# Kernel optimization log

Hardware: AMD Instinct MI355X
Metric: run time of the kernel (lower is better)

Reference implementation:

```python
import jax, jax.numpy as jnp
import numpy as np

B, T, E, H = 4, 512, 1024, 16
D = E // H  # 64
EPS = 1e-5  # torch LayerNorm default


def _ln(x, g, b):
    m = jnp.mean(x, axis=-1, keepdims=True)
    v = jnp.mean(jnp.square(x - m), axis=-1, keepdims=True)
    return (x - m) * jax.lax.rsqrt(v + EPS) * g + b


def _multihead(x, wq, wk, wv, g, b, mask):
    # x: [B,T,E]; wq/wk/wv: [H,E,D]; g,b: [H,D]; mask: [T,T] bool (causal)
    q = jnp.einsum('bte,hed->bhtd', x, wq)
    k = jnp.einsum('bte,hed->bhtd', x, wk)
    v = jnp.einsum('bte,hed->bhtd', x, wv)
    aff = jnp.einsum('bhtd,bhsd->bhts', q, k)  # NOTE: no 1/sqrt(d) scaling, as in source
    aff = jnp.where(mask, aff, -jnp.inf)
    p = jax.nn.softmax(aff, axis=-1)
    o = jnp.einsum('bhts,bhsd->bhtd', p, v)
    o = _ln(o, g[None, :, None, :], b[None, :, None, :])  # per-head LayerNorm over D
    o = o.transpose(0, 2, 1, 3).reshape(B, T, E)  # concat heads
    return x + o


def _ff(x, w1, b1, w2, b2, g, bb):
    h = jnp.maximum(jnp.einsum('bte,ef->btf', x, w1) + b1, 0.0)
    h = jnp.einsum('btf,fe->bte', h, w2) + b2
    h = _ln(h, g, bb)
    return x + h


def setup_inputs() -> dict:
    key = jax.random.key(0)
    ks = jax.random.split(key, 8)
    s = 0.02
    return {
        'x': jax.random.normal(ks[0], (B, T, E), jnp.float32),
        'mh_wq': jax.random.normal(ks[1], (5, H, E, D), jnp.float32) * s,
        'mh_wk': jax.random.normal(ks[2], (5, H, E, D), jnp.float32) * s,
        'mh_wv': jax.random.normal(ks[3], (5, H, E, D), jnp.float32) * s,
        'mh_g': jnp.ones((5, H, D), jnp.float32),
        'mh_b': jnp.zeros((5, H, D), jnp.float32),
        'ff_w1': jax.random.normal(ks[4], (4, E, 4 * E), jnp.float32) * s,
        'ff_b1': jnp.zeros((4, 4 * E), jnp.float32),
        'ff_w2': jax.random.normal(ks[5], (4, 4 * E, E), jnp.float32) * s,
        'ff_b2': jnp.zeros((4, E), jnp.float32),
        'ff_g': jnp.ones((4, E), jnp.float32),
        'ff_bb': jnp.zeros((4, E), jnp.float32),
        'lt_w': jax.random.normal(ks[6], (2 * E, E), jnp.float32) * s,
        'lt_b': jnp.zeros((E,), jnp.float32),
    }


def reference(x, mh_wq, mh_wk, mh_wv, mh_g, mh_b,
              ff_w1, ff_b1, ff_w2, ff_b2, ff_g, ff_bb, lt_w, lt_b):
    mask = jnp.tril(jnp.ones((T, T), dtype=bool))

    def mh(i, y):
        return _multihead(y, mh_wq[i], mh_wk[i], mh_wv[i], mh_g[i], mh_b[i], mask)

    def ff(i, y):
        return _ff(y, ff_w1[i], ff_b1[i], ff_w2[i], ff_b2[i], ff_g[i], ff_bb[i])

    def decoder(y):  # MultiHeadwithEncoder + FeedForward (param sets 4 / 3)
        return ff(3, mh(4, y))

    # head_one branch
    out_one = decoder(mh(0, x))
    # encoder branch: 3 EncoderBlocks (MultiHead + FeedForward each)
    out_two = x
    for i in range(3):
        out_two = ff(i, mh(1 + i, out_two))
    out_two = decoder(out_two)

    out = jnp.concatenate([out_one, out_two], axis=-1)
    out = jnp.einsum('btf,fe->bte', out, lt_w) + lt_b
    # input; the result is identical each time, so computing it once is faithful.
    return out
```

## Files before the change

kernel.cpp:

```cpp
#include <hip/hip_runtime.h>
#include <math.h>

#define Bb 4
#define Tt 512
#define Ee 1024
#define Hh 16
#define Dd 64
#define Ff 4096
#define Mm (Bb*Tt)
static constexpr float EPS = 1e-5f;

typedef __attribute__((ext_vector_type(8))) short short8;
typedef __attribute__((ext_vector_type(4))) float f32x4;
typedef unsigned short u16;
typedef _Float16 f16;
typedef __attribute__((ext_vector_type(8))) _Float16 f16x8;

__device__ __forceinline__ u16 f2bf(float f) {
  unsigned u = __builtin_bit_cast(unsigned, f);
  return (u16)((u + 0x7fffu + ((u >> 16) & 1u)) >> 16);
}
__device__ __forceinline__ float bf2f(u16 h) {
  unsigned u = (unsigned)h << 16;
  return __builtin_bit_cast(float, u);
}
__device__ __forceinline__ void gload16(const void* g, void* l) {
  __builtin_amdgcn_global_load_lds(
      (const __attribute__((address_space(1))) unsigned int*)g,
      (__attribute__((address_space(3))) unsigned int*)l, 16, 0, 0);
}

__global__ __launch_bounds__(256)
void gemm_f16_128(const f16* __restrict__ A, const f16* __restrict__ W,
                  const float* __restrict__ bias,
                  f16* __restrict__ C, int ldc, int K)
{
  __shared__ f16 AS[128][32], BS[128][32];
  const int tid = threadIdx.x;
  const int lane = tid & 63, w = tid >> 6;
  const int wr = w >> 1, wc = w & 1;
  const int lhi = lane >> 4, llo = lane & 15;
  const int n0 = blockIdx.x * 128, m0 = blockIdx.y * 128;
  const int s_row = tid >> 2, s_ko = (tid & 3) * 8;

  f32x4 acc[4][4] = {};

  for (int k0 = 0; k0 < K; k0 += 32) {
#pragma unroll
    for (int i = 0; i < 2; ++i) {
      const int row = s_row + i * 64;
      gload16(&A[(size_t)(m0 + row) * K + k0 + s_ko], &AS[row][s_ko]);
      gload16(&W[(size_t)(n0 + row) * K + k0 + s_ko], &BS[row][s_ko]);
    }
    __syncthreads();
    f16x8 af[4], bf[4];
#pragma unroll
    for (int f = 0; f < 4; ++f) {
      af[f] = *(const f16x8*)&AS[wr * 64 + f * 16 + llo][lhi * 8];
      bf[f] = *(const f16x8*)&BS[wc * 64 + f * 16 + llo][lhi * 8];
    }
#pragma unroll
    for (int m = 0; m < 4; ++m)
#pragma unroll
      for (int n = 0; n < 4; ++n)
        acc[m][n] = __builtin_amdgcn_mfma_f32_16x16x32_f16(af[m], bf[n], acc[m][n], 0, 0, 0);
    __syncthreads();
  }

#pragma unroll
  for (int n = 0; n < 4; ++n) {
    const int col = n0 + wc * 64 + n * 16 + llo;
    const float bv = bias[col];
#pragma unroll
    for (int m = 0; m < 4; ++m) {
      const int rbase = m0 + wr * 64 + m * 16 + lhi * 4;
#pragma unroll
      for (int j = 0; j < 4; ++j) {
        float v = fmaxf(acc[m][n][j] + bv, 0.f);
        C[(size_t)(rbase + j) * ldc + col] = (f16)v;
      }
    }
  }
}

template<bool CONCAT>
__global__ __launch_bounds__(256)
void gemm_f16_1p(const f16* __restrict__ A, const f16* __restrict__ A2,
                 const f16* __restrict__ W,
                 float* __restrict__ Cf, float* __restrict__ Cf1,
                 int ldc, int K)
{
  __shared__ f16 AS[2][64][32], BS[2][128][32];
  const int tid = threadIdx.x;
  const int lane = tid & 63, w = tid >> 6;
  const int wr = w >> 1, wc = w & 1;
  const int lhi = lane >> 4, llo = lane & 15;
  const int n0 = blockIdx.x * 128;
  const int m0 = blockIdx.y * 64;
  const int half = K >> 1;
  const int kbeg = blockIdx.z * half;
  const int nt = half / 32;
  if (blockIdx.z == 1) Cf = Cf1;

  const int s_row = tid >> 2, s_ko = (tid & 3) * 8;

  auto stage = [&](int k0, int buf) {
    const int gk = k0 + s_ko;
    const f16* s = A;
    size_t g;
    if (CONCAT) {
      if (gk < Ee) { g = (size_t)(m0 + s_row) * Ee + gk; }
      else { g = (size_t)(m0 + s_row) * Ee + (gk - Ee); s = A2; }
    } else {
      g = (size_t)(m0 + s_row) * K + gk;
    }
    gload16(&s[g], &AS[buf][s_row][s_ko]);
#pragma unroll
    for (int i = 0; i < 2; ++i)
      gload16(&W[(size_t)(n0 + s_row + i * 64) * K + gk], &BS[buf][s_row + i * 64][s_ko]);
  };

  f32x4 acc[2][4] = {};
  stage(kbeg, 0);
  __syncthreads();
  int cur = 0;
  for (int t = 0; t < nt; ++t) {
    if (t + 1 < nt) stage(kbeg + (t + 1) * 32, cur ^ 1);
    f16x8 af[2], bf[4];
#pragma unroll
    for (int m = 0; m < 2; ++m)
      af[m] = *(const f16x8*)&AS[cur][wr * 32 + m * 16 + llo][lhi * 8];
#pragma unroll
    for (int n = 0; n < 4; ++n)
      bf[n] = *(const f16x8*)&BS[cur][wc * 64 + n * 16 + llo][lhi * 8];
#pragma unroll
    for (int m = 0; m < 2; ++m)
#pragma unroll
      for (int n = 0; n < 4; ++n)
        acc[m][n] = __builtin_amdgcn_mfma_f32_16x16x32_f16(af[m], bf[n], acc[m][n], 0, 0, 0);
    __syncthreads();
    cur ^= 1;
  }

#pragma unroll
  for (int n = 0; n < 4; ++n) {
    const int col = n0 + wc * 64 + n * 16 + llo;
#pragma unroll
    for (int m = 0; m < 2; ++m) {
      const int rbase = m0 + wr * 32 + m * 16 + lhi * 4;
#pragma unroll
      for (int j = 0; j < 4; ++j)
        Cf[(size_t)(rbase + j) * ldc + col] = acc[m][n][j];
    }
  }
}

__global__ __launch_bounds__(256)
void gemm_qkv(const f16* __restrict__ Ah_g, const f16* __restrict__ Al_g,
              const f16* __restrict__ Wh, const f16* __restrict__ Wl,
              float* __restrict__ Cq, float* __restrict__ Ck, float* __restrict__ Cv)
{
  __shared__ f16 AhS[2][64][32], AlS[2][64][32];
  __shared__ f16 BhS[2][128][32], BlS[2][128][32];
  const int tid = threadIdx.x;
  const int lane = tid & 63, w = tid >> 6;
  const int wr = w >> 1, wc = w & 1;
  const int lhi = lane >> 4, llo = lane & 15;
  const int sec = blockIdx.x >> 3;
  const int n0 = (blockIdx.x & 7) * 128;
  Wh += (size_t)sec << 20;
  Wl += (size_t)sec << 20;
  float* Cf = (sec == 0) ? Cq : (sec == 1) ? Ck : Cv;
  const int m0 = blockIdx.y * 64;
  const int s_row = tid >> 2, s_ko = (tid & 3) * 8;

  auto stage = [&](int k0, int buf) {
    const size_t g = (size_t)(m0 + s_row) * Ee + k0 + s_ko;
    gload16(&Ah_g[g], &AhS[buf][s_row][s_ko]);
    gload16(&Al_g[g], &AlS[buf][s_row][s_ko]);
#pragma unroll
    for (int i = 0; i < 2; ++i) {
      size_t gb = (size_t)(n0 + s_row + i * 64) * Ee + k0 + s_ko;
      gload16(&Wh[gb], &BhS[buf][s_row + i * 64][s_ko]);
      gload16(&Wl[gb], &BlS[buf][s_row + i * 64][s_ko]);
    }
  };

  f32x4 acc[2][4] = {};
  stage(0, 0);
  __syncthreads();
  int cur = 0;
  for (int t = 0; t < Ee / 32; ++t) {
    if (t + 1 < Ee / 32) stage((t + 1) * 32, cur ^ 1);
    f16x8 ah[2], al[2], bh[4], bl[4];
#pragma unroll
    for (int m = 0; m < 2; ++m) {
      ah[m] = *(const f16x8*)&AhS[cur][wr * 32 + m * 16 + llo][lhi * 8];
      al[m] = *(const f16x8*)&AlS[cur][wr * 32 + m * 16 + llo][lhi * 8];
    }
#pragma unroll
    for (int n = 0; n < 4; ++n) {
      bh[n] = *(const f16x8*)&BhS[cur][wc * 64 + n * 16 + llo][lhi * 8];
      bl[n] = *(const f16x8*)&BlS[cur][wc * 64 + n * 16 + llo][lhi * 8];
    }
#pragma unroll
    for (int m = 0; m < 2; ++m)
#pragma unroll
      for (int n = 0; n < 4; ++n) {
        acc[m][n] = __builtin_amdgcn_mfma_f32_16x16x32_f16(ah[m], bh[n], acc[m][n], 0, 0, 0);
        acc[m][n] = __builtin_amdgcn_mfma_f32_16x16x32_f16(ah[m], bl[n], acc[m][n], 0, 0, 0);
        acc[m][n] = __builtin_amdgcn_mfma_f32_16x16x32_f16(al[m], bh[n], acc[m][n], 0, 0, 0);
      }
    __syncthreads();
    cur ^= 1;
  }

#pragma unroll
  for (int n = 0; n < 4; ++n) {
    const int col = n0 + wc * 64 + n * 16 + llo;
#pragma unroll
    for (int m = 0; m < 2; ++m) {
      const int rbase = m0 + wr * 32 + m * 16 + lhi * 4;
#pragma unroll
      for (int j = 0; j < 4; ++j)
        Cf[(size_t)(rbase + j) * Ee + col] = acc[m][n][j];
    }
  }
}

__global__ __launch_bounds__(256)
void attn_ms(const float* __restrict__ Q, const float* __restrict__ Kp,
             const float* __restrict__ V, float* __restrict__ O)
{
  __shared__ u16 Ksh[64][72], Ksl[64][72];
  __shared__ u16 Vsh[64][72], Vsl[64][72];
  __shared__ u16 Pwh[4][16][72], Pwl[4][16][72];
  const int tid = threadIdx.x;
  const int lane = tid & 63, w = tid >> 6;
  const int lhi = lane >> 4, llo = lane & 15;
  const int q0 = blockIdx.x * 64;
  const int bh = blockIdx.y;
  const size_t base = (size_t)(bh >> 4) * Tt * Ee + (size_t)(bh & 15) * Dd;

  short8 qh[2], ql[2];
#pragma unroll
  for (int ks = 0; ks < 2; ++ks) {
    const float* qsrc = &Q[base + (size_t)(q0 + w * 16 + llo) * Ee + ks * 32 + lhi * 8];
    float4 a = *(const float4*)qsrc, b2 = *(const float4*)(qsrc + 4);
    float f[8] = {a.x, a.y, a.z, a.w, b2.x, b2.y, b2.z, b2.w};
#pragma unroll
    for (int j = 0; j < 8; ++j) {
      u16 h = f2bf(f[j]);
      qh[ks][j] = (short)h;
      ql[ks][j] = (short)f2bf(f[j] - bf2f(h));
    }
  }

  f32x4 oacc[4] = {};
  float m_run[4], l_run[4];
#pragma unroll
  for (int j = 0; j < 4; ++j) { m_run[j] = -INFINITY; l_run[j] = 0.f; }

  for (int s0 = 0; s0 <= q0; s0 += 64) {
#pragma unroll
    for (int pass = 0; pass < 2; ++pass) {
      int c = tid + 256 * pass;
      int row = c >> 3, d0 = (c & 7) * 8;
      const float* ksrc = &Kp[base + (size_t)(s0 + row) * Ee + d0];
      const float* vsrc = &V[base + (size_t)(s0 + row) * Ee + d0];
      float4 ka = *(const float4*)ksrc, kb2 = *(const float4*)(ksrc + 4);
      float4 va = *(const float4*)vsrc, vb2 = *(const float4*)(vsrc + 4);
      float kf[8] = {ka.x, ka.y, ka.z, ka.w, kb2.x, kb2.y, kb2.z, kb2.w};
      float vf[8] = {va.x, va.y, va.z, va.w, vb2.x, vb2.y, vb2.z, vb2.w};
      short8 khv, klv;
#pragma unroll
      for (int j = 0; j < 8; ++j) {
        u16 h = f2bf(kf[j]);
        khv[j] = (short)h;
        klv[j] = (short)f2bf(kf[j] - bf2f(h));
      }
      *(short8*)&Ksh[row][d0] = khv;
      *(short8*)&Ksl[row][d0] = klv;
#pragma unroll
      for (int j = 0; j < 8; ++j) {
        u16 h = f2bf(vf[j]);
        Vsh[d0 + j][row] = h;
        Vsl[d0 + j][row] = f2bf(vf[j] - bf2f(h));
      }
    }
    __syncthreads();

    f32x4 sacc[4] = {};
#pragma unroll
    for (int ks = 0; ks < 2; ++ks)
#pragma unroll
      for (int n = 0; n < 4; ++n) {
        short8 kh = *(const short8*)&Ksh[n * 16 + llo][ks * 32 + lhi * 8];
        short8 kl = *(const short8*)&Ksl[n * 16 + llo][ks * 32 + lhi * 8];
        sacc[n] = __builtin_amdgcn_mfma_f32_16x16x32_bf16(qh[ks], kh, sacc[n], 0, 0, 0);
        sacc[n] = __builtin_amdgcn_mfma_f32_16x16x32_bf16(qh[ks], kl, sacc[n], 0, 0, 0);
        sacc[n] = __builtin_amdgcn_mfma_f32_16x16x32_bf16(ql[ks], kh, sacc[n], 0, 0, 0);
      }

    if (s0 == q0) {
#pragma unroll
      for (int n = 0; n < 4; ++n)
#pragma unroll
        for (int j = 0; j < 4; ++j)
          if (n * 16 + llo > w * 16 + lhi * 4 + j) sacc[n][j] = -INFINITY;
    }

    float scj[4];
#pragma unroll
    for (int j = 0; j < 4; ++j) {
      float mt = fmaxf(fmaxf(sacc[0][j], sacc[1][j]), fmaxf(sacc[2][j], sacc[3][j]));
#pragma unroll
      for (int off = 1; off < 16; off <<= 1) mt = fmaxf(mt, __shfl_xor(mt, off));
      float mn = fmaxf(m_run[j], mt);
      scj[j] = __expf(m_run[j] - mn);
      m_run[j] = mn;
      float rs = 0.f;
#pragma unroll
      for (int n = 0; n < 4; ++n) {
        float pp = __expf(sacc[n][j] - mn);
        sacc[n][j] = pp;
        rs += pp;
      }
#pragma unroll
      for (int off = 1; off < 16; off <<= 1) rs += __shfl_xor(rs, off);
      l_run[j] = l_run[j] * scj[j] + rs;
    }

#pragma unroll
    for (int n = 0; n < 4; ++n)
#pragma unroll
      for (int j = 0; j < 4; ++j) {
        float pp = sacc[n][j];
        u16 h = f2bf(pp);
        Pwh[w][lhi * 4 + j][n * 16 + llo] = h;
        Pwl[w][lhi * 4 + j][n * 16 + llo] = f2bf(pp - bf2f(h));
      }
#pragma unroll
    for (int df = 0; df < 4; ++df)
#pragma unroll
      for (int j = 0; j < 4; ++j)
        oacc[df][j] *= scj[j];

#pragma unroll
    for (int ks = 0; ks < 2; ++ks) {
      short8 ph = *(const short8*)&Pwh[w][llo][ks * 32 + lhi * 8];
      short8 pl = *(const short8*)&Pwl[w][llo][ks * 32 + lhi * 8];
#pragma unroll
      for (int df = 0; df < 4; ++df) {
        short8 vh = *(const short8*)&Vsh[df * 16 + llo][ks * 32 + lhi * 8];
        short8 vl = *(const short8*)&Vsl[df * 16 + llo][ks * 32 + lhi * 8];
        oacc[df] = __builtin_amdgcn_mfma_f32_16x16x32_bf16(ph, vh, oacc[df], 0, 0, 0);
        oacc[df] = __builtin_amdgcn_mfma_f32_16x16x32_bf16(ph, vl, oacc[df], 0, 0, 0);
        oacc[df] = __builtin_amdgcn_mfma_f32_16x16x32_bf16(pl, vh, oacc[df], 0, 0, 0);
      }
    }
    __syncthreads();
  }

#pragma unroll
  for (int j = 0; j < 4; ++j) {
    float inv = 1.f / l_run[j];
#pragma unroll
    for (int df = 0; df < 4; ++df)
      O[base + (size_t)(q0 + w * 16 + lhi * 4 + j) * Ee + df * 16 + llo] =
          oacc[df][j] * inv;
  }
}

__global__ __launch_bounds__(256)
void attn_ln_res(const float* __restrict__ O, const float* __restrict__ Yin,
                 const float* __restrict__ g, const float* __restrict__ bta,
                 float* __restrict__ Yout, f16* __restrict__ Yh, f16* __restrict__ Yl)
{
  const int tid = threadIdx.x;
  const int w = (blockIdx.x << 2) + (tid >> 6);
  const int lane = tid & 63;
  const int m = w >> 4;
  const int h = w & 15;
  const size_t idx = (size_t)m * Ee + h * Dd + lane;
  float x = O[idx];
  float s = x, s2 = x * x;
#pragma unroll
  for (int off = 1; off < 64; off <<= 1) {
    s  += __shfl_xor(s, off);
    s2 += __shfl_xor(s2, off);
  }
  float mean = s * (1.f / 64.f);
  float var  = s2 * (1.f / 64.f) - mean * mean;
  float inv  = rsqrtf(var + EPS);
  float r = Yin[idx] + (x - mean) * inv * g[h * Dd + lane] + bta[h * Dd + lane];
  Yout[idx] = r;
  f16 hh = (f16)r;
  Yh[idx] = hh;
  Yl[idx] = (f16)(r - (float)hh);
}

__global__ __launch_bounds__(256)
void ff_ln_res(const float* __restrict__ T0, const float* __restrict__ T1,
               const float* __restrict__ b2,
               const float* __restrict__ Yin, const float* __restrict__ g,
               const float* __restrict__ bb,
               float* __restrict__ Yout, f16* __restrict__ Yh, f16* __restrict__ Yl)
{
  __shared__ float red[8];
  const int m = blockIdx.x;
  const int tid = threadIdx.x;
  const size_t basep = (size_t)m * Ee;
  float4 xa = *(const float4*)&T0[basep + (tid << 2)];
  float4 xb = *(const float4*)&T1[basep + (tid << 2)];
  float4 bv2 = *(const float4*)&b2[tid << 2];
  float xv[4] = {xa.x + xb.x + bv2.x, xa.y + xb.y + bv2.y,
                 xa.z + xb.z + bv2.z, xa.w + xb.w + bv2.w};
  float s  = xv[0] + xv[1] + xv[2] + xv[3];
  float s2 = xv[0]*xv[0] + xv[1]*xv[1] + xv[2]*xv[2] + xv[3]*xv[3];
#pragma unroll
  for (int off = 1; off < 64; off <<= 1) {
    s  += __shfl_xor(s, off);
    s2 += __shfl_xor(s2, off);
  }
  const int wid = tid >> 6;
  if ((tid & 63) == 0) { red[wid] = s; red[4 + wid] = s2; }
  __syncthreads();
  s  = red[0] + red[1] + red[2] + red[3];
  s2 = red[4] + red[5] + red[6] + red[7];
  float mean = s * (1.f / Ee);
  float var  = s2 * (1.f / Ee) - mean * mean;
  float inv  = rsqrtf(var + EPS);
  float4 y  = *(const float4*)&Yin[basep + (tid << 2)];
  float4 gg = *(const float4*)&g[tid << 2];
  float4 bv = *(const float4*)&bb[tid << 2];
  float gga[4] = {gg.x, gg.y, gg.z, gg.w};
  float bva[4] = {bv.x, bv.y, bv.z, bv.w};
  float ya[4] = {y.x, y.y, y.z, y.w};
  float o[4];
#pragma unroll
  for (int j = 0; j < 4; ++j) {
    o[j] = ya[j] + (xv[j] - mean) * inv * gga[j] + bva[j];
    f16 hh = (f16)o[j];
    Yh[basep + (tid << 2) + j] = hh;
    Yl[basep + (tid << 2) + j] = (f16)(o[j] - (float)hh);
  }
  *(float4*)&Yout[basep + (tid << 2)] = *(float4*)o;
}

__global__ __launch_bounds__(256)
void add2_bias(const float* __restrict__ p0, const float* __restrict__ p1,
               const float* __restrict__ b, float* __restrict__ out)
{
  const size_t i = ((size_t)blockIdx.x * 256 + threadIdx.x) * 4;
  const int col = (int)(i & (Ee - 1));
  float4 a = *(const float4*)&p0[i];
  float4 c = *(const float4*)&p1[i];
  float4 bb = *(const float4*)&b[col];
  float4 o;
  o.x = a.x + c.x + bb.x; o.y = a.y + c.y + bb.y;
  o.z = a.z + c.z + bb.z; o.w = a.w + c.w + bb.w;
  *(float4*)&out[i] = o;
}

__global__ __launch_bounds__(256)
void split_act(const float* __restrict__ in, f16* __restrict__ oh, f16* __restrict__ ol)
{
  const size_t i = ((size_t)blockIdx.x * 256 + threadIdx.x) * 4;
  float4 v = *(const float4*)&in[i];
  float f[4] = {v.x, v.y, v.z, v.w};
#pragma unroll
  for (int j = 0; j < 4; ++j) {
    f16 h = (f16)f[j];
    oh[i + j] = h;
    ol[i + j] = (f16)(f[j] - (float)h);
  }
}

__global__ __launch_bounds__(256)
void cvtT_f16(const float* __restrict__ in, f16* __restrict__ outp, int R, int C)
{
  __shared__ float tile[32][33];
  const int c0 = blockIdx.x * 32, r0 = blockIdx.y * 32;
  const int tid = threadIdx.x;
  const int ir = tid >> 3, ic = (tid & 7) * 4;
  float4 v = *(const float4*)&in[(size_t)(r0 + ir) * C + c0 + ic];
  tile[ir][ic] = v.x; tile[ir][ic + 1] = v.y;
  tile[ir][ic + 2] = v.z; tile[ir][ic + 3] = v.w;
  __syncthreads();
  const int oc = tid >> 3, orr = (tid & 7) * 4;
  const size_t ob = (size_t)(c0 + oc) * R + r0 + orr;
#pragma unroll
  for (int j = 0; j < 4; ++j)
    outp[ob + j] = (f16)tile[orr + j][oc];
}

__global__ __launch_bounds__(256)
void cvtT_qkv(const float* __restrict__ wq, const float* __restrict__ wk,
              const float* __restrict__ wv, f16* __restrict__ out_h,
              f16* __restrict__ out_l)
{
  __shared__ float tile[32][33];
  const int z = blockIdx.z, sec = z >> 4, hh = z & 15;
  const float* in = (sec == 0) ? wq : (sec == 1) ? wk : wv;
  const size_t zi = (size_t)hh * Ee * Dd;
  const size_t zo = ((size_t)sec << 20) + (size_t)hh * Ee * Dd;
  const int c0 = blockIdx.x * 32, r0 = blockIdx.y * 32;
  const int tid = threadIdx.x;
  const int ir = tid >> 3, ic = (tid & 7) * 4;
  float4 v = *(const float4*)&in[zi + (size_t)(r0 + ir) * Dd + c0 + ic];
  tile[ir][ic] = v.x; tile[ir][ic + 1] = v.y;
  tile[ir][ic + 2] = v.z; tile[ir][ic + 3] = v.w;
  __syncthreads();
  const int oc = tid >> 3, orr = (tid & 7) * 4;
  const size_t ob = zo + (size_t)(c0 + oc) * Ee + r0 + orr;
#pragma unroll
  for (int j = 0; j < 4; ++j) {
    float f = tile[orr + j][oc];
    f16 h = (f16)f;
    out_h[ob + j] = h;
    out_l[ob + j] = (f16)(f - (float)h);
  }
}

extern "C" void kernel_launch(void* const* d_in, const int* in_sizes, int n_in,
                              void* d_out, int out_size, void* d_ws, size_t ws_size,
                              hipStream_t stream)
{
  const float* x     = (const float*)d_in[0];
  const float* mh_wq = (const float*)d_in[1];
  const float* mh_wk = (const float*)d_in[2];
  const float* mh_wv = (const float*)d_in[3];
  const float* mh_g  = (const float*)d_in[4];
  const float* mh_b  = (const float*)d_in[5];
  const float* ff_w1 = (const float*)d_in[6];
  const float* ff_b1 = (const float*)d_in[7];
  const float* ff_w2 = (const float*)d_in[8];
  const float* ff_b2 = (const float*)d_in[9];
  const float* ff_g  = (const float*)d_in[10];
  const float* ff_bb = (const float*)d_in[11];
  const float* lt_w  = (const float*)d_in[12];
  const float* lt_b  = (const float*)d_in[13];
  float* out = (float*)d_out;

  const size_t ME = (size_t)Mm * Ee;
  char* p = (char*)d_ws;
  auto alloc = [&](size_t bytes) { void* r = (void*)p; p += (bytes + 255) & ~(size_t)255; return r; };
  float* bufA  = (float*)alloc(ME * 4);
  f16*   bufAh = (f16*)alloc(ME * 2);
  f16*   bufAl = (f16*)alloc(ME * 2);
  float* bufB  = (float*)alloc(ME * 4);
  f16*   bufBh = (f16*)alloc(ME * 2);
  f16*   bufBl = (f16*)alloc(ME * 2);
  f16*   wt_h  = (f16*)alloc((size_t)Ff * Ee * 2);
  f16*   wt_l  = (f16*)alloc((size_t)Ff * Ee * 2);
  float* reg   = (float*)alloc((size_t)10 * 1024 * 1024 * 4);
  float* qb    = reg;
  float* kb    = reg + 2 * 1024 * 1024;
  float* vb    = reg + 4 * 1024 * 1024;
  float* ob    = reg + 6 * 1024 * 1024;
  f16*   hid   = (f16*)reg;
  float* tmp   = reg + 8 * 1024 * 1024;

  auto mh = [&](int i, const float* srcF, const f16* srcH, const f16* srcL,
                float* dstF, f16* dstH, f16* dstL) {
    const size_t wo = (size_t)i * Hh * Ee * Dd;
    cvtT_qkv<<<dim3(Dd / 32, Ee / 32, 48), 256, 0, stream>>>(
        mh_wq + wo, mh_wk + wo, mh_wv + wo, wt_h, wt_l);
    gemm_qkv<<<dim3(24, Mm / 64), 256, 0, stream>>>(
        srcH, srcL, wt_h, wt_l, qb, kb, vb);
    attn_ms<<<dim3(Tt / 64, Bb * Hh), 256, 0, stream>>>(qb, kb, vb, ob);
    attn_ln_res<<<dim3(Mm * Hh / 4), 256, 0, stream>>>(
        ob, srcF, mh_g + (size_t)i * Hh * Dd, mh_b + (size_t)i * Hh * Dd, dstF, dstH, dstL);
  };
  auto ff = [&](int i, const float* srcF, const f16* srcH,
                float* dstF, f16* dstH, f16* dstL, float* tmp1) {
    cvtT_f16<<<dim3(Ff / 32, Ee / 32), 256, 0, stream>>>(ff_w1 + (size_t)i * Ee * Ff, wt_h, Ee, Ff);
    gemm_f16_128<<<dim3(Ff / 128, Mm / 128), 256, 0, stream>>>(
        srcH, wt_h, ff_b1 + (size_t)i * Ff, hid, Ff, Ee);
    cvtT_f16<<<dim3(Ee / 32, Ff / 32), 256, 0, stream>>>(ff_w2 + (size_t)i * Ff * Ee, wt_h, Ff, Ee);
    gemm_f16_1p<false><<<dim3(Ee / 128, Mm / 64, 2), 256, 0, stream>>>(
        hid, nullptr, wt_h, tmp, tmp1, Ee, Ff);
    ff_ln_res<<<dim3(Mm), 256, 0, stream>>>(
        tmp, tmp1, ff_b2 + (size_t)i * Ee,
        srcF, ff_g + (size_t)i * Ee, ff_bb + (size_t)i * Ee, dstF, dstH, dstL);
  };

  split_act<<<dim3(ME / 1024), 256, 0, stream>>>(x, bufAh, bufAl);
  mh(0, x, bufAh, bufAl, bufA, bufAh, bufAl);
  mh(4, bufA, bufAh, bufAl, bufA, bufAh, bufAl);
  ff(3, bufA, bufAh, bufA, bufAh, bufAl, bufB);

  split_act<<<dim3(ME / 1024), 256, 0, stream>>>(x, bufBh, bufBl);
  mh(1, x, bufBh, bufBl, bufB, bufBh, bufBl);
  ff(0, bufB, bufBh, bufB, bufBh, bufBl, bufA);
  mh(2, bufB, bufBh, bufBl, bufB, bufBh, bufBl);
  ff(1, bufB, bufBh, bufB, bufBh, bufBl, bufA);
  mh(3, bufB, bufBh, bufBl, bufB, bufBh, bufBl);
  ff(2, bufB, bufBh, bufB, bufBh, bufBl, bufA);
  mh(4, bufB, bufBh, bufBl, bufB, bufBh, bufBl);
  ff(3, bufB, bufBh, bufB, bufBh, bufBl, bufA);

  cvtT_f16<<<dim3(Ee / 32, 2 * Ee / 32), 256, 0, stream>>>(lt_w, wt_h, 2 * Ee, Ee);
  gemm_f16_1p<true><<<dim3(Ee / 128, Mm / 64, 2), 256, 0, stream>>>(
      bufAh, bufBh, wt_h, bufA, bufB, Ee, 2 * Ee);
  add2_bias<<<dim3(ME / 1024), 256, 0, stream>>>(bufA, bufB, lt_b, out);
}
```

Measured before the change: 1.149 ms.

## Emit split-f16 Q/K and single-f16 V from QKV GEMM; drop extra MFMAs

```diff
diff --git a/kernel.cpp b/kernel.cpp
--- a/kernel.cpp
+++ b/kernel.cpp
@@ -10,20 +10,10 @@
 #define Mm (Bb*Tt)
 static constexpr float EPS = 1e-5f;
 
-typedef __attribute__((ext_vector_type(8))) short short8;
 typedef __attribute__((ext_vector_type(4))) float f32x4;
-typedef unsigned short u16;
 typedef _Float16 f16;
 typedef __attribute__((ext_vector_type(8))) _Float16 f16x8;
 
-__device__ __forceinline__ u16 f2bf(float f) {
-  unsigned u = __builtin_bit_cast(unsigned, f);
-  return (u16)((u + 0x7fffu + ((u >> 16) & 1u)) >> 16);
-}
-__device__ __forceinline__ float bf2f(u16 h) {
-  unsigned u = (unsigned)h << 16;
-  return __builtin_bit_cast(float, u);
-}
 __device__ __forceinline__ void gload16(const void* g, void* l) {
   __builtin_amdgcn_global_load_lds(
       (const __attribute__((address_space(1))) unsigned int*)g,
@@ -158,7 +148,9 @@
 __global__ __launch_bounds__(256)
 void gemm_qkv(const f16* __restrict__ Ah_g, const f16* __restrict__ Al_g,
               const f16* __restrict__ Wh, const f16* __restrict__ Wl,
-              float* __restrict__ Cq, float* __restrict__ Ck, float* __restrict__ Cv)
+              f16* __restrict__ Qh, f16* __restrict__ Ql,
+              f16* __restrict__ Kh, f16* __restrict__ Kl,
+              f16* __restrict__ Vv)
 {
   __shared__ f16 AhS[2][64][32], AlS[2][64][32];
   __shared__ f16 BhS[2][128][32], BlS[2][128][32];
@@ -167,22 +159,22 @@
   const int wr = w >> 1, wc = w & 1;
   const int lhi = lane >> 4, llo = lane & 15;
   const int sec = blockIdx.x >> 3;
+  const bool three = (sec < 2);
   const int n0 = (blockIdx.x & 7) * 128;
   Wh += (size_t)sec << 20;
   Wl += (size_t)sec << 20;
-  float* Cf = (sec == 0) ? Cq : (sec == 1) ? Ck : Cv;
   const int m0 = blockIdx.y * 64;
   const int s_row = tid >> 2, s_ko = (tid & 3) * 8;
 
   auto stage = [&](int k0, int buf) {
     const size_t g = (size_t)(m0 + s_row) * Ee + k0 + s_ko;
     gload16(&Ah_g[g], &AhS[buf][s_row][s_ko]);
-    gload16(&Al_g[g], &AlS[buf][s_row][s_ko]);
+    if (three) gload16(&Al_g[g], &AlS[buf][s_row][s_ko]);
 #pragma unroll
     for (int i = 0; i < 2; ++i) {
       size_t gb = (size_t)(n0 + s_row + i * 64) * Ee + k0 + s_ko;
       gload16(&Wh[gb], &BhS[buf][s_row + i * 64][s_ko]);
-      gload16(&Wl[gb], &BlS[buf][s_row + i * 64][s_ko]);
+      if (three) gload16(&Wl[gb], &BlS[buf][s_row + i * 64][s_ko]);
     }
   };
 
@@ -192,25 +184,36 @@
   int cur = 0;
   for (int t = 0; t < Ee / 32; ++t) {
     if (t + 1 < Ee / 32) stage((t + 1) * 32, cur ^ 1);
-    f16x8 ah[2], al[2], bh[4], bl[4];
-#pragma unroll
-    for (int m = 0; m < 2; ++m) {
+    f16x8 ah[2], bh[4];
+#pragma unroll
+    for (int m = 0; m < 2; ++m)
       ah[m] = *(const f16x8*)&AhS[cur][wr * 32 + m * 16 + llo][lhi * 8];
-      al[m] = *(const f16x8*)&AlS[cur][wr * 32 + m * 16 + llo][lhi * 8];
-    }
-#pragma unroll
-    for (int n = 0; n < 4; ++n) {
+#pragma unroll
+    for (int n = 0; n < 4; ++n)
       bh[n] = *(const f16x8*)&BhS[cur][wc * 64 + n * 16 + llo][lhi * 8];
-      bl[n] = *(const f16x8*)&BlS[cur][wc * 64 + n * 16 + llo][lhi * 8];
-    }
-#pragma unroll
-    for (int m = 0; m < 2; ++m)
-#pragma unroll
-      for (int n = 0; n < 4; ++n) {
-        acc[m][n] = __builtin_amdgcn_mfma_f32_16x16x32_f16(ah[m], bh[n], acc[m][n], 0, 0, 0);
-        acc[m][n] = __builtin_amdgcn_mfma_f32_16x16x32_f16(ah[m], bl[n], acc[m][n], 0, 0, 0);
-        acc[m][n] = __builtin_amdgcn_mfma_f32_16x16x32_f16(al[m], bh[n], acc[m][n], 0, 0, 0);
-      }
+    if (three) {
+      f16x8 al[2], bl[4];
+#pragma unroll
+      for (int m = 0; m < 2; ++m)
+        al[m] = *(const f16x8*)&AlS[cur][wr * 32 + m * 16 + llo][lhi * 8];
+#pragma unroll
+      for (int n = 0; n < 4; ++n)
+        bl[n] = *(const f16x8*)&BlS[cur][wc * 64 + n * 16 + llo][lhi * 8];
+#pragma unroll
+      for (int m = 0; m < 2; ++m)
+#pragma unroll
+        for (int n = 0; n < 4; ++n) {
+          acc[m][n] = __builtin_amdgcn_mfma_f32_16x16x32_f16(ah[m], bh[n], acc[m][n], 0, 0, 0);
+          acc[m][n] = __builtin_amdgcn_mfma_f32_16x16x32_f16(ah[m], bl[n], acc[m][n], 0, 0, 0);
+          acc[m][n] = __builtin_amdgcn_mfma_f32_16x16x32_f16(al[m], bh[n], acc[m][n], 0, 0, 0);
+        }
+    } else {
+#pragma unroll
+      for (int m = 0; m < 2; ++m)
+#pragma unroll
+        for (int n = 0; n < 4; ++n)
+          acc[m][n] = __builtin_amdgcn_mfma_f32_16x16x32_f16(ah[m], bh[n], acc[m][n], 0, 0, 0);
+    }
     __syncthreads();
     cur ^= 1;
   }
@@ -222,19 +225,33 @@
     for (int m = 0; m < 2; ++m) {
       const int rbase = m0 + wr * 32 + m * 16 + lhi * 4;
 #pragma unroll
-      for (int j = 0; j < 4; ++j)
-        Cf[(size_t)(rbase + j) * Ee + col] = acc[m][n][j];
-    }
-  }
-}
-
-__global__ __launch_bounds__(256)
-void attn_ms(const float* __restrict__ Q, const float* __restrict__ Kp,
-             const float* __restrict__ V, float* __restrict__ O)
-{
-  __shared__ u16 Ksh[64][72], Ksl[64][72];
-  __shared__ u16 Vsh[64][72], Vsl[64][72];
-  __shared__ u16 Pwh[4][16][72], Pwl[4][16][72];
+      for (int j = 0; j < 4; ++j) {
+        const float v = acc[m][n][j];
+        const size_t idx = (size_t)(rbase + j) * Ee + col;
+        if (sec == 0) {
+          f16 h = (f16)v;
+          Qh[idx] = h;
+          Ql[idx] = (f16)(v - (float)h);
+        } else if (sec == 1) {
+          f16 h = (f16)v;
+          Kh[idx] = h;
+          Kl[idx] = (f16)(v - (float)h);
+        } else {
+          Vv[idx] = (f16)v;
+        }
+      }
+    }
+  }
+}
+
+__global__ __launch_bounds__(256)
+void attn_ms(const f16* __restrict__ Qh_g, const f16* __restrict__ Ql_g,
+             const f16* __restrict__ Kh_g, const f16* __restrict__ Kl_g,
+             const f16* __restrict__ Vv_g, float* __restrict__ O)
+{
+  __shared__ f16 Ksh[64][72], Ksl[64][72];
+  __shared__ f16 Vs[64][72];
+  __shared__ f16 Pw[4][16][72];
   const int tid = threadIdx.x;
   const int lane = tid & 63, w = tid >> 6;
   const int lhi = lane >> 4, llo = lane & 15;
@@ -242,18 +259,12 @@
   const int bh = blockIdx.y;
   const size_t base = (size_t)(bh >> 4) * Tt * Ee + (size_t)(bh & 15) * Dd;
 
-  short8 qh[2], ql[2];
+  f16x8 qfh[2], qfl[2];
 #pragma unroll
   for (int ks = 0; ks < 2; ++ks) {
-    const float* qsrc = &Q[base + (size_t)(q0 + w * 16 + llo) * Ee + ks * 32 + lhi * 8];
-    float4 a = *(const float4*)qsrc, b2 = *(const float4*)(qsrc + 4);
-    float f[8] = {a.x, a.y, a.z, a.w, b2.x, b2.y, b2.z, b2.w};
-#pragma unroll
-    for (int j = 0; j < 8; ++j) {
-      u16 h = f2bf(f[j]);
-      qh[ks][j] = (short)h;
-      ql[ks][j] = (short)f2bf(f[j] - bf2f(h));
-    }
+    const size_t qoff = base + (size_t)(q0 + w * 16 + llo) * Ee + ks * 32 + lhi * 8;
+    qfh[ks] = *(const f16x8*)&Qh_g[qoff];
+    qfl[ks] = *(const f16x8*)&Ql_g[qoff];
   }
 
   f32x4 oacc[4] = {};
@@ -266,27 +277,14 @@
     for (int pass = 0; pass < 2; ++pass) {
       int c = tid + 256 * pass;
       int row = c >> 3, d0 = (c & 7) * 8;
-      const float* ksrc = &Kp[base + (size_t)(s0 + row) * Ee + d0];
-      const float* vsrc = &V[base + (size_t)(s0 + row) * Ee + d0];
-      float4 ka = *(const float4*)ksrc, kb2 = *(const float4*)(ksrc + 4);
-      float4 va = *(const float4*)vsrc, vb2 = *(const float4*)(vsrc + 4);
-      float kf[8] = {ka.x, ka.y, ka.z, ka.w, kb2.x, kb2.y, kb2.z, kb2.w};
-      float vf[8] = {va.x, va.y, va.z, va.w, vb2.x, vb2.y, vb2.z, vb2.w};
-      short8 khv, klv;
-#pragma unroll
-      for (int j = 0; j < 8; ++j) {
-        u16 h = f2bf(kf[j]);
-        khv[j] = (short)h;
-        klv[j] = (short)f2bf(kf[j] - bf2f(h));
-      }
-      *(short8*)&Ksh[row][d0] = khv;
-      *(short8*)&Ksl[row][d0] = klv;
-#pragma unroll
-      for (int j = 0; j < 8; ++j) {
-        u16 h = f2bf(vf[j]);
-        Vsh[d0 + j][row] = h;
-        Vsl[d0 + j][row] = f2bf(vf[j] - bf2f(h));
-      }
+      const size_t g = base + (size_t)(s0 + row) * Ee + d0;
+      f16x8 kh = *(const f16x8*)&Kh_g[g];
+      f16x8 kl = *(const f16x8*)&Kl_g[g];
+      f16x8 vf = *(const f16x8*)&Vv_g[g];
+      *(f16x8*)&Ksh[row][d0] = kh;
+      *(f16x8*)&Ksl[row][d0] = kl;
+#pragma unroll
+      for (int j = 0; j < 8; ++j) Vs[d0 + j][row] = vf[j];
     }
     __syncthreads();
 
@@ -295,11 +293,11 @@
     for (int ks = 0; ks < 2; ++ks)
 #pragma unroll
       for (int n = 0; n < 4; ++n) {
-        short8 kh = *(const short8*)&Ksh[n * 16 + llo][ks * 32 + lhi * 8];
-        short8 kl = *(const short8*)&Ksl[n * 16 + llo][ks * 32 + lhi * 8];
-        sacc[n] = __builtin_amdgcn_mfma_f32_16x16x32_bf16(qh[ks], kh, sacc[n], 0, 0, 0);
-        sacc[n] = __builtin_amdgcn_mfma_f32_16x16x32_bf16(qh[ks], kl, sacc[n], 0, 0, 0);
-        sacc[n] = __builtin_amdgcn_mfma_f32_16x16x32_bf16(ql[ks], kh, sacc[n], 0, 0, 0);
+        f16x8 kfh = *(const f16x8*)&Ksh[n * 16 + llo][ks * 32 + lhi * 8];
+        f16x8 kfl = *(const f16x8*)&Ksl[n * 16 + llo][ks * 32 + lhi * 8];
+        sacc[n] = __builtin_amdgcn_mfma_f32_16x16x32_f16(qfh[ks], kfh, sacc[n], 0, 0, 0);
+        sacc[n] = __builtin_amdgcn_mfma_f32_16x16x32_f16(qfh[ks], kfl, sacc[n], 0, 0, 0);
+        sacc[n] = __builtin_amdgcn_mfma_f32_16x16x32_f16(qfl[ks], kfh, sacc[n], 0, 0, 0);
       }
 
     if (s0 == q0) {
@@ -334,12 +332,8 @@
 #pragma unroll
     for (int n = 0; n < 4; ++n)
 #pragma unroll
-      for (int j = 0; j < 4; ++j) {
-        float pp = sacc[n][j];
-        u16 h = f2bf(pp);
-        Pwh[w][lhi * 4 + j][n * 16 + llo] = h;
-        Pwl[w][lhi * 4 + j][n * 16 + llo] = f2bf(pp - bf2f(h));
-      }
+      for (int j = 0; j < 4; ++j)
+        Pw[w][lhi * 4 + j][n * 16 + llo] = (f16)sacc[n][j];
 #pragma unroll
     for (int df = 0; df < 4; ++df)
 #pragma unroll
@@ -348,15 +342,11 @@
 
 #pragma unroll
     for (int ks = 0; ks < 2; ++ks) {
-      short8 ph = *(const short8*)&Pwh[w][llo][ks * 32 + lhi * 8];
-      short8 pl = *(const short8*)&Pwl[w][llo][ks * 32 + lhi * 8];
+      f16x8 pf = *(const f16x8*)&Pw[w][llo][ks * 32 + lhi * 8];
 #pragma unroll
       for (int df = 0; df < 4; ++df) {
-        short8 vh = *(const short8*)&Vsh[df * 16 + llo][ks * 32 + lhi * 8];
-        short8 vl = *(const short8*)&Vsl[df * 16 + llo][ks * 32 + lhi * 8];
-        oacc[df] = __builtin_amdgcn_mfma_f32_16x16x32_bf16(ph, vh, oacc[df], 0, 0, 0);
-        oacc[df] = __builtin_amdgcn_mfma_f32_16x16x32_bf16(ph, vl, oacc[df], 0, 0, 0);
-        oacc[df] = __builtin_amdgcn_mfma_f32_16x16x32_bf16(pl, vh, oacc[df], 0, 0, 0);
+        f16x8 vfr = *(const f16x8*)&Vs[df * 16 + llo][ks * 32 + lhi * 8];
+        oacc[df] = __builtin_amdgcn_mfma_f32_16x16x32_f16(pf, vfr, oacc[df], 0, 0, 0);
       }
     }
     __syncthreads();
@@ -555,10 +545,12 @@
   f16*   wt_h  = (f16*)alloc((size_t)Ff * Ee * 2);
   f16*   wt_l  = (f16*)alloc((size_t)Ff * Ee * 2);
   float* reg   = (float*)alloc((size_t)10 * 1024 * 1024 * 4);
-  float* qb    = reg;
-  float* kb    = reg + 2 * 1024 * 1024;
-  float* vb    = reg + 4 * 1024 * 1024;
-  float* ob    = reg + 6 * 1024 * 1024;
+  f16*   qh_   = (f16*)reg;
+  f16*   ql_   = qh_ + ME;
+  f16*   kh_   = qh_ + 2 * ME;
+  f16*   kl_   = qh_ + 3 * ME;
+  f16*   vv_   = qh_ + 4 * ME;
+  float* ob    = reg + 5 * 1024 * 1024;
   f16*   hid   = (f16*)reg;
   float* tmp   = reg + 8 * 1024 * 1024;
 
@@ -568,8 +560,8 @@
     cvtT_qkv<<<dim3(Dd / 32, Ee / 32, 48), 256, 0, stream>>>(
         mh_wq + wo, mh_wk + wo, mh_wv + wo, wt_h, wt_l);
     gemm_qkv<<<dim3(24, Mm / 64), 256, 0, stream>>>(
-        srcH, srcL, wt_h, wt_l, qb, kb, vb);
-    attn_ms<<<dim3(Tt / 64, Bb * Hh), 256, 0, stream>>>(qb, kb, vb, ob);
+        srcH, srcL, wt_h, wt_l, qh_, ql_, kh_, kl_, vv_);
+    attn_ms<<<dim3(Tt / 64, Bb * Hh), 256, 0, stream>>>(qh_, ql_, kh_, kl_, vv_, ob);
     attn_ln_res<<<dim3(Mm * Hh / 4), 256, 0, stream>>>(
         ob, srcF, mh_g + (size_t)i * Hh * Dd, mh_b + (size_t)i * Hh * Dd, dstF, dstH, dstL);
   };
```

Result: faster. 1.039 ms (-9.6%).
